# Performance work log

Hardware: AMD Instinct MI355X
Metric: run time of the kernel (lower is better)

## Reference

```python
import jax, jax.numpy as jnp
import numpy as np

EMBED = 768
HEADS = 12
HEAD_DIM = EMBED // HEADS
HIDDEN = 4 * EMBED


def layer_norm(x, gamma, beta, eps=1e-5):
    mu = jnp.mean(x, axis=-1, keepdims=True)
    var = jnp.var(x, axis=-1, keepdims=True)
    return (x - mu) * jax.lax.rsqrt(var + eps) * gamma + beta


def setup_inputs() -> dict:
    key = jax.random.key(0)
    ks = jax.random.split(key, 10)
    B, N, C = 64, 577, EMBED
    s_in = 1.0 / np.sqrt(C)
    s_hid = 1.0 / np.sqrt(HIDDEN)
    return {
        "x": jax.random.normal(ks[0], (B, N, C), jnp.float32),
        "ln1_g": jnp.ones((C,), jnp.float32),
        "ln1_b": jnp.zeros((C,), jnp.float32),
        "w_qkv": jax.random.normal(ks[1], (C, 3 * C), jnp.float32) * s_in,  # no bias (qkv_bias=False)
        "w_proj": jax.random.normal(ks[2], (C, C), jnp.float32) * s_in,
        "b_proj": jnp.zeros((C,), jnp.float32),
        "ln2_g": jnp.ones((C,), jnp.float32),
        "ln2_b": jnp.zeros((C,), jnp.float32),
        "w_fc1": jax.random.normal(ks[3], (C, HIDDEN), jnp.float32) * s_in,
        "b_fc1": jnp.zeros((HIDDEN,), jnp.float32),
        "w_fc2": jax.random.normal(ks[4], (HIDDEN, C), jnp.float32) * s_hid,
        "b_fc2": jnp.zeros((C,), jnp.float32),
    }


def reference(x, ln1_g, ln1_b, w_qkv, w_proj, b_proj, ln2_g, ln2_b, w_fc1, b_fc1, w_fc2, b_fc2):
    B, N, C = x.shape
    # --- attention branch (pre-norm) ---
    h = layer_norm(x, ln1_g, ln1_b)
    qkv = (h @ w_qkv).reshape(B, N, 3, HEADS, HEAD_DIM)
    q = jnp.transpose(qkv[:, :, 0], (0, 2, 1, 3))  # [B,H,N,D]
    k = jnp.transpose(qkv[:, :, 1], (0, 2, 1, 3))
    v = jnp.transpose(qkv[:, :, 2], (0, 2, 1, 3))
    scale = HEAD_DIM ** -0.5
    att = jax.nn.softmax(jnp.einsum("bhnd,bhmd->bhnm", q, k) * scale, axis=-1)
    o = jnp.einsum("bhnm,bhmd->bhnd", att, v)
    o = jnp.transpose(o, (0, 2, 1, 3)).reshape(B, N, C)
    x = x + (o @ w_proj + b_proj)
    # --- MLP branch (pre-norm) ---
    h = layer_norm(x, ln2_g, ln2_b)
    h = jax.nn.gelu(h @ w_fc1 + b_fc1, approximate=False)
    x = x + (h @ w_fc2 + b_fc2)
    return x
```

## Files before the change

kernel.cpp:

```cpp
#include <hip/hip_runtime.h>
#include <hip/hip_bf16.h>
#include <math.h>

using bf16 = __hip_bfloat16;
typedef __attribute__((ext_vector_type(8))) short short8;
typedef __attribute__((ext_vector_type(4))) float f32x4;

#define NSEQ   577
#define NBATCH 64
#define NTOK   36928
#define MPAD   37120
#define NHEADS 12
#define HDIM   64
#define NP     640
#define CEMB   768
#define CHID   3072
#define NBH    (NBATCH*NHEADS)

__device__ __forceinline__ bf16 f2bf(float v){ return __float2bfloat16(v); }

__device__ __forceinline__ float gelu_f(float x) {
    float x3 = x * x * x;
    float y = 1.5957691216057308f * (x + 0.044715f * x3);
    float e = __expf(y);
    float t = 1.0f - 2.0f / (e + 1.0f);
    return 0.5f * x * (1.0f + t);
}

#define GLOAD_LDS16(gaddr, laddr) \
  __builtin_amdgcn_global_load_lds((__attribute__((address_space(1))) const void*)(gaddr), \
                                   (__attribute__((address_space(3))) void*)(laddr), 16, 0, 0)

__global__ __launch_bounds__(256) void transpose_w(const float* __restrict__ src,
                                                   bf16* __restrict__ dst, int R, int C) {
    long idx = (long)blockIdx.x * 256 + threadIdx.x;
    long total = (long)R * C;
    if (idx < total) {
        int r = (int)(idx / C);
        int c = (int)(idx - (long)r * C);
        dst[(long)c * R + r] = f2bf(src[idx]);
    }
}

__global__ __launch_bounds__(256) void ln_kernel(const float* __restrict__ x,
                                                 const float* __restrict__ gamma,
                                                 const float* __restrict__ beta,
                                                 bf16* __restrict__ out) {
    int row = blockIdx.x;
    const float* xr = x + (size_t)row * CEMB;
    int tid = threadIdx.x;
    float v0 = xr[tid], v1 = xr[tid + 256], v2 = xr[tid + 512];
    float s = v0 + v1 + v2;
    #pragma unroll
    for (int o = 32; o > 0; o >>= 1) s += __shfl_down(s, o);
    __shared__ float red[4];
    if ((tid & 63) == 0) red[tid >> 6] = s;
    __syncthreads();
    float mean = (red[0] + red[1] + red[2] + red[3]) * (1.0f / CEMB);
    float d0 = v0 - mean, d1 = v1 - mean, d2 = v2 - mean;
    float q = d0*d0 + d1*d1 + d2*d2;
    #pragma unroll
    for (int o = 32; o > 0; o >>= 1) q += __shfl_down(q, o);
    __shared__ float red2[4];
    if ((tid & 63) == 0) red2[tid >> 6] = q;
    __syncthreads();
    float var = (red2[0] + red2[1] + red2[2] + red2[3]) * (1.0f / CEMB);
    float rs = rsqrtf(var + 1e-5f);
    bf16* orow = out + (size_t)row * CEMB;
    orow[tid]       = f2bf(d0 * rs * gamma[tid]       + beta[tid]);
    orow[tid + 256] = f2bf(d1 * rs * gamma[tid + 256] + beta[tid + 256]);
    orow[tid + 512] = f2bf(d2 * rs * gamma[tid + 512] + beta[tid + 512]);
}

__global__ __launch_bounds__(256) void flash_attn(const bf16* __restrict__ qg,
                                                  const bf16* __restrict__ kg,
                                                  const bf16* __restrict__ vtg,
                                                  bf16* __restrict__ og) {
    const int tid = threadIdx.x, lane = tid & 63, w = tid >> 6;
    const int fr = lane & 15, fh = lane >> 4;
    const int bh = blockIdx.y;
    const int q0 = blockIdx.x * 128;
    const int wr = w * 32;

    __shared__ bf16 Ks[64 * 64];
    __shared__ bf16 Vs[64 * 64];
    __shared__ bf16 Ps[128 * 64];

    const bf16* qb = qg  + (size_t)bh * NP * HDIM;
    const bf16* kb = kg  + (size_t)bh * NP * HDIM;
    const bf16* vb = vtg + (size_t)bh * HDIM * NP;

    const int swz  = (fr & 7) << 3;
    const int scol = (((lane & 7) ^ (lane >> 3)) << 3);
    const int srow = lane >> 3;

    short8 qa[2][2];
    #pragma unroll
    for (int mi = 0; mi < 2; mi++)
        #pragma unroll
        for (int ks = 0; ks < 2; ks++)
            qa[mi][ks] = *reinterpret_cast<const short8*>(
                qb + (size_t)(q0 + wr + mi * 16 + fr) * HDIM + ks * 32 + fh * 8);

    f32x4 od[2][4] = {};
    float m_run[2][4], l_run[2][4];
    #pragma unroll
    for (int mi = 0; mi < 2; mi++)
        #pragma unroll
        for (int r = 0; r < 4; r++) { m_run[mi][r] = -1e30f; l_run[mi][r] = 0.f; }

    for (int t = 0; t < NP / 64; t++) {
        const int kb0 = t * 64;
        __syncthreads();
        GLOAD_LDS16(kb + (size_t)(kb0 + w * 8 + srow) * HDIM + scol,      Ks + w * 512);
        GLOAD_LDS16(kb + (size_t)(kb0 + 32 + w * 8 + srow) * HDIM + scol, Ks + 2048 + w * 512);
        GLOAD_LDS16(vb + (size_t)(w * 8 + srow) * NP + kb0 + scol,        Vs + w * 512);
        GLOAD_LDS16(vb + (size_t)(32 + w * 8 + srow) * NP + kb0 + scol,   Vs + 2048 + w * 512);
        __syncthreads();

        f32x4 sacc[2][4] = {};
        short8 kf[4][2];
        #pragma unroll
        for (int n = 0; n < 4; n++)
            #pragma unroll
            for (int ks = 0; ks < 2; ks++)
                kf[n][ks] = *reinterpret_cast<const short8*>(
                    &Ks[(n * 16 + fr) * 64 + ((ks * 32 + fh * 8) ^ swz)]);
        __builtin_amdgcn_s_setprio(1);
        #pragma unroll
        for (int mi = 0; mi < 2; mi++)
            #pragma unroll
            for (int n = 0; n < 4; n++)
                #pragma unroll
                for (int ks = 0; ks < 2; ks++)
                    sacc[mi][n] = __builtin_amdgcn_mfma_f32_16x16x32_bf16(qa[mi][ks], kf[n][ks], sacc[mi][n], 0, 0, 0);
        __builtin_amdgcn_s_setprio(0);

        #pragma unroll
        for (int mi = 0; mi < 2; mi++) {
            float sv[4][4];
            float tm[4] = {-1e30f, -1e30f, -1e30f, -1e30f};
            #pragma unroll
            for (int n = 0; n < 4; n++) {
                int col = kb0 + n * 16 + fr;
                bool valid = col < NSEQ;
                #pragma unroll
                for (int r = 0; r < 4; r++) {
                    float s = sacc[mi][n][r];
                    sv[n][r] = valid ? s : -1e30f;
                    tm[r] = fmaxf(tm[r], sv[n][r]);
                }
            }
            #pragma unroll
            for (int r = 0; r < 4; r++) {
                #pragma unroll
                for (int o = 1; o < 16; o <<= 1) tm[r] = fmaxf(tm[r], __shfl_xor(tm[r], o));
                float mo = m_run[mi][r];
                if (tm[r] - mo > 8.f) {
                    float sc = __expf(mo - tm[r]);
                    mo = tm[r];
                    m_run[mi][r] = mo;
                    l_run[mi][r] *= sc;
                    #pragma unroll
                    for (int n2 = 0; n2 < 4; n2++) od[mi][n2][r] *= sc;
                }
                float ps = 0.f;
                #pragma unroll
                for (int n = 0; n < 4; n++) {
                    float e = __expf(sv[n][r] - mo);
                    sv[n][r] = e; ps += e;
                }
                #pragma unroll
                for (int o = 1; o < 16; o <<= 1) ps += __shfl_xor(ps, o);
                l_run[mi][r] += ps;
            }
            #pragma unroll
            for (int n = 0; n < 4; n++)
                #pragma unroll
                for (int r = 0; r < 4; r++)
                    Ps[(wr + mi * 16 + fh * 4 + r) * 64 +
                       ((n * 16 + fr) ^ (((fh * 4 + r) & 7) << 3))] = f2bf(sv[n][r]);
        }
        __syncthreads();

        short8 pa[2][2], vf[4][2];
        #pragma unroll
        for (int mi = 0; mi < 2; mi++)
            #pragma unroll
            for (int ks = 0; ks < 2; ks++)
                pa[mi][ks] = *reinterpret_cast<const short8*>(
                    &Ps[(wr + mi * 16 + fr) * 64 + ((ks * 32 + fh * 8) ^ swz)]);
        #pragma unroll
        for (int n2 = 0; n2 < 4; n2++)
            #pragma unroll
            for (int ks = 0; ks < 2; ks++)
                vf[n2][ks] = *reinterpret_cast<const short8*>(
                    &Vs[(n2 * 16 + fr) * 64 + ((ks * 32 + fh * 8) ^ swz)]);
        __builtin_amdgcn_s_setprio(1);
        #pragma unroll
        for (int mi = 0; mi < 2; mi++)
            #pragma unroll
            for (int n2 = 0; n2 < 4; n2++)
                #pragma unroll
                for (int ks = 0; ks < 2; ks++)
                    od[mi][n2] = __builtin_amdgcn_mfma_f32_16x16x32_bf16(pa[mi][ks], vf[n2][ks], od[mi][n2], 0, 0, 0);
        __builtin_amdgcn_s_setprio(0);
    }

    const int b = bh / NHEADS, hh = bh - b * NHEADS;
    #pragma unroll
    for (int mi = 0; mi < 2; mi++)
        #pragma unroll
        for (int r = 0; r < 4; r++) {
            int qrow = q0 + wr + mi * 16 + fh * 4 + r;
            if (qrow < NSEQ) {
                float inv = 1.f / l_run[mi][r];
                #pragma unroll
                for (int n2 = 0; n2 < 4; n2++)
                    og[((size_t)(b * NSEQ + qrow)) * CEMB + hh * HDIM + n2 * 16 + fr] =
                        f2bf(od[mi][n2][r] * inv);
            }
        }
}

#define MODE_QKV  1
#define MODE_PROJ 3
#define MODE_FC1  4
#define MODE_FC2  5

struct GemmParams {
    const bf16* A;
    const bf16* Bt;
    int M, N, K;
    int Mreal;
    float* Cf;
    bf16* Cb;
    const float* bias;
    const float* resid;
    bf16* qb; bf16* kb; bf16* vtb;
};

template<int MODE>
__global__ __launch_bounds__(512, 2) void gemm256(GemmParams p) {
    __shared__ bf16 AsBuf[2][256 * 64];
    __shared__ bf16 BsBuf[2][256 * 64];
    const int tid  = threadIdx.x;
    const int lane = tid & 63;
    const int w    = tid >> 6;

    const int gx = gridDim.x, gy = gridDim.y;
    const int nwg = gx * gy;
    const int orig = blockIdx.y * gx + blockIdx.x;
    const int q8 = nwg >> 3, r8 = nwg & 7;
    const int xcd = orig & 7, oid = orig >> 3;
    const int lin2 = ((xcd < r8) ? xcd * (q8 + 1) : r8 * (q8 + 1) + (xcd - r8) * q8) + oid;
    const int bm = (lin2 / gy) * 256;
    const int bn = (lin2 % gy) * 256;

    const int Kd = p.K;
    const int wm = w >> 2, wn = w & 3;
    const int wr = wm * 128, wc = wn * 64;
    const int fr = lane & 15;
    const int fk = (lane >> 4) * 8;

    const int sr = w * 8 + (lane >> 3);
    const int sc = (lane & 7) * 8;
    const bf16* aS[4]; const bf16* bS[4];
    #pragma unroll
    for (int s = 0; s < 4; s++) {
        aS[s] = p.A  + (size_t)(bm + s * 64 + sr) * Kd + sc;
        bS[s] = p.Bt + (size_t)(bn + s * 64 + sr) * Kd + sc;
    }

    f32x4 acc[8][4] = {};
    bf16 *Ac = AsBuf[0], *An = AsBuf[1], *Bc = BsBuf[0], *Bn = BsBuf[1];

    auto stage = [&](bf16* Ad, bf16* Bd) {
        #pragma unroll
        for (int s = 0; s < 4; s++) {
            GLOAD_LDS16(aS[s], Ad + (size_t)(s * 8 + w) * 512);
            GLOAD_LDS16(bS[s], Bd + (size_t)(s * 8 + w) * 512);
            aS[s] += 64; bS[s] += 64;
        }
    };
    auto compute = [&](const bf16* Ad, const bf16* Bd) {
        #pragma unroll
        for (int ks = 0; ks < 2; ks++) {
            short8 b[4];
            #pragma unroll
            for (int n = 0; n < 4; n++)
                b[n] = *reinterpret_cast<const short8*>(&Bd[(wc + n * 16 + fr) * 64 + ks * 32 + fk]);
            #pragma unroll
            for (int m = 0; m < 8; m++) {
                short8 a = *reinterpret_cast<const short8*>(&Ad[(wr + m * 16 + fr) * 64 + ks * 32 + fk]);
                #pragma unroll
                for (int n = 0; n < 4; n++)
                    acc[m][n] = __builtin_amdgcn_mfma_f32_16x16x32_bf16(a, b[n], acc[m][n], 0, 0, 0);
            }
        }
    };

    const int T = Kd >> 6;
    stage(Ac, Bc);
    __syncthreads();
    for (int t = 1; t < T; ++t) {
        stage(An, Bn);
        compute(Ac, Bc);
        __syncthreads();
        bf16* tp;
        tp = Ac; Ac = An; An = tp;
        tp = Bc; Bc = Bn; Bn = tp;
    }
    compute(Ac, Bc);

    const int fq = (lane >> 4) * 4;
    const int colw = bn + wc;

    if (MODE == MODE_QKV) {
        const int which = colw / CEMB;
        const int hh = (colw - which * CEMB) >> 6;
        const float scl = (which == 0) ? 0.125f : 1.0f;
        #pragma unroll
        for (int m = 0; m < 8; m++)
        #pragma unroll
        for (int r = 0; r < 4; r++) {
            int row = bm + wr + m * 16 + fq + r;
            if (row < p.Mreal) {
                int b2 = row / NSEQ;
                int n2 = row - b2 * NSEQ;
                size_t bh = (size_t)b2 * NHEADS + hh;
                if (which == 0) {
                    bf16* dst = p.qb + (bh * NP + n2) * HDIM + fr;
                    #pragma unroll
                    for (int n = 0; n < 4; n++) dst[n * 16] = f2bf(acc[m][n][r] * scl);
                } else if (which == 1) {
                    bf16* dst = p.kb + (bh * NP + n2) * HDIM + fr;
                    #pragma unroll
                    for (int n = 0; n < 4; n++) dst[n * 16] = f2bf(acc[m][n][r]);
                } else {
                    bf16* dst = p.vtb + (bh * HDIM + fr) * NP + n2;
                    #pragma unroll
                    for (int n = 0; n < 4; n++) dst[(size_t)n * 16 * NP] = f2bf(acc[m][n][r]);
                }
            }
        }
    } else if (MODE == MODE_FC1) {
        const float* bp = p.bias + colw + fr;
        float bb[4];
        #pragma unroll
        for (int n = 0; n < 4; n++) bb[n] = bp[n * 16];
        #pragma unroll
        for (int m = 0; m < 8; m++)
        #pragma unroll
        for (int r = 0; r < 4; r++) {
            int row = bm + wr + m * 16 + fq + r;
            if (row < p.Mreal) {
                bf16* crow = p.Cb + (size_t)row * p.N + colw + fr;
                #pragma unroll
                for (int n = 0; n < 4; n++)
                    crow[n * 16] = f2bf(gelu_f(acc[m][n][r] + bb[n]));
            }
        }
    } else {
        const float* bp = p.bias + colw + fr;
        float bb[4];
        #pragma unroll
        for (int n = 0; n < 4; n++) bb[n] = bp[n * 16];
        #pragma unroll
        for (int m = 0; m < 8; m++)
        #pragma unroll
        for (int r = 0; r < 4; r++) {
            int row = bm + wr + m * 16 + fq + r;
            if (row < p.Mreal) {
                float* crow = p.Cf + (size_t)row * p.N + colw + fr;
                const float* rrow = p.resid + (size_t)row * p.N + colw + fr;
                #pragma unroll
                for (int n = 0; n < 4; n++)
                    crow[n * 16] = acc[m][n][r] + bb[n] + rrow[n * 16];
            }
        }
    }
}

extern "C" void kernel_launch(void* const* d_in, const int* in_sizes, int n_in,
                              void* d_out, int out_size, void* d_ws, size_t ws_size,
                              hipStream_t stream) {
    const float* x      = (const float*)d_in[0];
    const float* ln1_g  = (const float*)d_in[1];
    const float* ln1_b  = (const float*)d_in[2];
    const float* w_qkv  = (const float*)d_in[3];
    const float* w_proj = (const float*)d_in[4];
    const float* b_proj = (const float*)d_in[5];
    const float* ln2_g  = (const float*)d_in[6];
    const float* ln2_b  = (const float*)d_in[7];
    const float* w_fc1  = (const float*)d_in[8];
    const float* b_fc1  = (const float*)d_in[9];
    const float* w_fc2  = (const float*)d_in[10];
    const float* b_fc2  = (const float*)d_in[11];
    float* out = (float*)d_out;

    char* ws = (char*)d_ws;
    auto al = [](size_t b){ return (b + 255) & ~(size_t)255; };
    size_t off = 0;
    auto take = [&](size_t b)->char* { char* p = ws + off; off += al(b); return p; };

    bf16* wqkvT  = (bf16*)take((size_t)2304 * 768 * 2);
    bf16* wprojT = (bf16*)take((size_t)768 * 768 * 2);
    bf16* wfc1T  = (bf16*)take((size_t)3072 * 768 * 2);
    bf16* wfc2T  = (bf16*)take((size_t)768 * 3072 * 2);
    bf16* h      = (bf16*)take((size_t)MPAD * CEMB * 2);
    bf16* o      = (bf16*)take((size_t)MPAD * CEMB * 2);
    size_t fixedEnd = off;

    const size_t qkvB = (size_t)NBH * NP * HDIM * 2;
    bf16* q_c  = (bf16*)(ws + fixedEnd);
    bf16* k_c  = (bf16*)(ws + fixedEnd + qkvB);
    bf16* vT_c = (bf16*)(ws + fixedEnd + 2 * qkvB);
    bf16* g_c  = (bf16*)(ws + fixedEnd);

    transpose_w<<<(768 * 2304 + 255) / 256, 256, 0, stream>>>(w_qkv, wqkvT, 768, 2304);
    transpose_w<<<(768 * 768 + 255) / 256, 256, 0, stream>>>(w_proj, wprojT, 768, 768);
    transpose_w<<<(768 * 3072 + 255) / 256, 256, 0, stream>>>(w_fc1, wfc1T, 768, 3072);
    transpose_w<<<(3072 * 768 + 255) / 256, 256, 0, stream>>>(w_fc2, wfc2T, 3072, 768);

    ln_kernel<<<NTOK, 256, 0, stream>>>(x, ln1_g, ln1_b, h);

    {
        GemmParams p{};
        p.A = h; p.Bt = wqkvT;
        p.M = MPAD; p.N = 3 * CEMB; p.K = CEMB; p.Mreal = NTOK;
        p.qb = q_c; p.kb = k_c; p.vtb = vT_c;
        gemm256<MODE_QKV><<<dim3(MPAD / 256, 3 * CEMB / 256), 512, 0, stream>>>(p);
    }

    flash_attn<<<dim3(NP / 128, NBH), 256, 0, stream>>>(q_c, k_c, vT_c, o);

    {
        GemmParams p{};
        p.A = o; p.Bt = wprojT;
        p.M = MPAD; p.N = CEMB; p.K = CEMB; p.Mreal = NTOK;
        p.Cf = out; p.bias = b_proj; p.resid = x;
        gemm256<MODE_PROJ><<<dim3(MPAD / 256, CEMB / 256), 512, 0, stream>>>(p);
    }

    ln_kernel<<<NTOK, 256, 0, stream>>>(out, ln2_g, ln2_b, h);

    {
        GemmParams p{};
        p.A = h; p.Bt = wfc1T;
        p.M = MPAD; p.N = CHID; p.K = CEMB; p.Mreal = NTOK;
        p.Cb = g_c; p.bias = b_fc1;
        gemm256<MODE_FC1><<<dim3(MPAD / 256, CHID / 256), 512, 0, stream>>>(p);
    }

    {
        GemmParams p{};
        p.A = g_c; p.Bt = wfc2T;
        p.M = MPAD; p.N = CEMB; p.K = CHID; p.Mreal = NTOK;
        p.Cf = out; p.bias = b_fc2; p.resid = out;
        gemm256<MODE_FC2><<<dim3(MPAD / 256, CEMB / 256), 512, 0, stream>>>(p);
    }
}
```

Baseline: 1.381 ms.

## Prefetch two K/V and GEMM tiles ahead with explicit vmcnt waits

Flash attention now double-buffers its K/V shared-memory tiles and keeps two tiles of global-to-LDS loads in flight. Each wave waits on vmcnt for its own loads, then a raw s_barrier publishes the tile, which replaces __syncthreads. The block-wide barrier between writing P and reading it is dropped for an lgkmcnt wait, since each wave only reads back its own P rows. The GEMM main loop gets the same two-deep prefetch with vmcnt(8) waits. This hides global-load latency and removes barrier stalls, but relies on exact vmcnt counting, which breaks if the number of loads per stage ever changes.

```diff
diff --git a/kernel.cpp b/kernel.cpp
--- a/kernel.cpp
+++ b/kernel.cpp
@@ -82,8 +82,8 @@
     const int q0 = blockIdx.x * 128;
     const int wr = w * 32;
 
-    __shared__ bf16 Ks[64 * 64];
-    __shared__ bf16 Vs[64 * 64];
+    __shared__ bf16 Ks[2][64 * 64];
+    __shared__ bf16 Vs[2][64 * 64];
     __shared__ bf16 Ps[128 * 64];
 
     const bf16* qb = qg  + (size_t)bh * NP * HDIM;
@@ -101,6 +101,11 @@
         for (int ks = 0; ks < 2; ks++)
             qa[mi][ks] = *reinterpret_cast<const short8*>(
                 qb + (size_t)(q0 + wr + mi * 16 + fr) * HDIM + ks * 32 + fh * 8);
+    #pragma unroll
+    for (int mi = 0; mi < 2; mi++)
+        #pragma unroll
+        for (int ks = 0; ks < 2; ks++)
+            asm volatile("" : "+v"(qa[mi][ks]));
 
     f32x4 od[2][4] = {};
     float m_run[2][4], l_run[2][4];
@@ -109,15 +114,14 @@
         #pragma unroll
         for (int r = 0; r < 4; r++) { m_run[mi][r] = -1e30f; l_run[mi][r] = 0.f; }
 
-    for (int t = 0; t < NP / 64; t++) {
-        const int kb0 = t * 64;
-        __syncthreads();
-        GLOAD_LDS16(kb + (size_t)(kb0 + w * 8 + srow) * HDIM + scol,      Ks + w * 512);
-        GLOAD_LDS16(kb + (size_t)(kb0 + 32 + w * 8 + srow) * HDIM + scol, Ks + 2048 + w * 512);
-        GLOAD_LDS16(vb + (size_t)(w * 8 + srow) * NP + kb0 + scol,        Vs + w * 512);
-        GLOAD_LDS16(vb + (size_t)(32 + w * 8 + srow) * NP + kb0 + scol,   Vs + 2048 + w * 512);
-        __syncthreads();
-
+    auto stageKV = [&](int buf, int kb0) {
+        GLOAD_LDS16(kb + (size_t)(kb0 + w * 8 + srow) * HDIM + scol,      Ks[buf] + w * 512);
+        GLOAD_LDS16(kb + (size_t)(kb0 + 32 + w * 8 + srow) * HDIM + scol, Ks[buf] + 2048 + w * 512);
+        GLOAD_LDS16(vb + (size_t)(w * 8 + srow) * NP + kb0 + scol,        Vs[buf] + w * 512);
+        GLOAD_LDS16(vb + (size_t)(32 + w * 8 + srow) * NP + kb0 + scol,   Vs[buf] + 2048 + w * 512);
+    };
+
+    auto tileBody = [&](int buf, int kb0) {
         f32x4 sacc[2][4] = {};
         short8 kf[4][2];
         #pragma unroll
@@ -125,7 +129,7 @@
             #pragma unroll
             for (int ks = 0; ks < 2; ks++)
                 kf[n][ks] = *reinterpret_cast<const short8*>(
-                    &Ks[(n * 16 + fr) * 64 + ((ks * 32 + fh * 8) ^ swz)]);
+                    &Ks[buf][(n * 16 + fr) * 64 + ((ks * 32 + fh * 8) ^ swz)]);
         __builtin_amdgcn_s_setprio(1);
         #pragma unroll
         for (int mi = 0; mi < 2; mi++)
@@ -181,7 +185,8 @@
                     Ps[(wr + mi * 16 + fh * 4 + r) * 64 +
                        ((n * 16 + fr) ^ (((fh * 4 + r) & 7) << 3))] = f2bf(sv[n][r]);
         }
-        __syncthreads();
+        asm volatile("s_waitcnt lgkmcnt(0)" ::: "memory");
+        __builtin_amdgcn_sched_barrier(0);
 
         short8 pa[2][2], vf[4][2];
         #pragma unroll
@@ -195,7 +200,7 @@
             #pragma unroll
             for (int ks = 0; ks < 2; ks++)
                 vf[n2][ks] = *reinterpret_cast<const short8*>(
-                    &Vs[(n2 * 16 + fr) * 64 + ((ks * 32 + fh * 8) ^ swz)]);
+                    &Vs[buf][(n2 * 16 + fr) * 64 + ((ks * 32 + fh * 8) ^ swz)]);
         __builtin_amdgcn_s_setprio(1);
         #pragma unroll
         for (int mi = 0; mi < 2; mi++)
@@ -205,7 +210,21 @@
                 for (int ks = 0; ks < 2; ks++)
                     od[mi][n2] = __builtin_amdgcn_mfma_f32_16x16x32_bf16(pa[mi][ks], vf[n2][ks], od[mi][n2], 0, 0, 0);
         __builtin_amdgcn_s_setprio(0);
-    }
+    };
+
+    stageKV(0, 0);
+    stageKV(1, 64);
+    for (int t = 0; t < 9; ++t) {
+        asm volatile("s_waitcnt vmcnt(4)" ::: "memory");
+        __builtin_amdgcn_s_barrier();
+        tileBody(t & 1, t * 64);
+        asm volatile("s_waitcnt lgkmcnt(0)" ::: "memory");
+        __builtin_amdgcn_s_barrier();
+        if (t + 2 < 10) stageKV(t & 1, (t + 2) * 64);
+    }
+    asm volatile("s_waitcnt vmcnt(0)" ::: "memory");
+    __builtin_amdgcn_s_barrier();
+    tileBody(1, 9 * 64);
 
     const int b = bh / NHEADS, hh = bh - b * NHEADS;
     #pragma unroll
@@ -273,7 +292,6 @@
     }
 
     f32x4 acc[8][4] = {};
-    bf16 *Ac = AsBuf[0], *An = AsBuf[1], *Bc = BsBuf[0], *Bn = BsBuf[1];
 
     auto stage = [&](bf16* Ad, bf16* Bd) {
         #pragma unroll
@@ -301,17 +319,19 @@
     };
 
     const int T = Kd >> 6;
-    stage(Ac, Bc);
-    __syncthreads();
-    for (int t = 1; t < T; ++t) {
-        stage(An, Bn);
-        compute(Ac, Bc);
-        __syncthreads();
-        bf16* tp;
-        tp = Ac; Ac = An; An = tp;
-        tp = Bc; Bc = Bn; Bn = tp;
-    }
-    compute(Ac, Bc);
+    stage(AsBuf[0], BsBuf[0]);
+    stage(AsBuf[1], BsBuf[1]);
+    for (int t = 0; t < T - 1; ++t) {
+        asm volatile("s_waitcnt vmcnt(8)" ::: "memory");
+        __builtin_amdgcn_s_barrier();
+        compute(AsBuf[t & 1], BsBuf[t & 1]);
+        asm volatile("s_waitcnt lgkmcnt(0)" ::: "memory");
+        __builtin_amdgcn_s_barrier();
+        if (t + 2 < T) stage(AsBuf[t & 1], BsBuf[t & 1]);
+    }
+    asm volatile("s_waitcnt vmcnt(0)" ::: "memory");
+    __builtin_amdgcn_s_barrier();
+    compute(AsBuf[(T - 1) & 1], BsBuf[(T - 1) & 1]);
 
     const int fq = (lane >> 4) * 4;
     const int colw = bn + wc;
```

New measurement: 1.503 ms. 1.09x slower.
